# Kernel tuning notes

Hardware: AMD Instinct MI355X
Metric: run time of the kernel (lower is better)

## Reference

```python
import jax, jax.numpy as jnp
import numpy as np

NUM_EMBEDDINGS = 16384
EMBED_DIM = 256
COMMITMENT_COST = 0.25  # legacy=True: vq_loss = commit + beta * codebook


def setup_inputs() -> dict:
    key = jax.random.key(0)
    k1, k2, k3, k4 = jax.random.split(key, 4)
    z = jax.random.normal(k1, (8, 2048, EMBED_DIM), dtype=jnp.float32)
    # frozen codebook: normal(0, embedding_dim ** -0.5)
    codebook = jax.random.normal(k2, (NUM_EMBEDDINGS, EMBED_DIM), dtype=jnp.float32) * (EMBED_DIM ** -0.5)
    # learnable linear projection, torch default uniform init
    bound = 1.0 / np.sqrt(EMBED_DIM)
    proj_w = jax.random.uniform(k3, (EMBED_DIM, EMBED_DIM), dtype=jnp.float32, minval=-bound, maxval=bound)
    proj_b = jax.random.uniform(k4, (EMBED_DIM,), dtype=jnp.float32, minval=-bound, maxval=bound)
    return {"z": z, "codebook": codebook, "proj_w": proj_w, "proj_b": proj_b}


def reference(z, codebook, proj_w, proj_b):
    B, T, D = z.shape
    # projected codebook (the only learned part of the quantizer)
    quant_codebook = codebook @ proj_w.T + proj_b  # [K, D]
    z_flat = z.reshape(-1, D)  # [N, D]
    # squared L2 distances: ||z||^2 + ||c||^2 - 2 z.c
    dists = (
        jnp.sum(z_flat * z_flat, axis=1, keepdims=True)
        + jnp.sum(quant_codebook * quant_codebook, axis=1)
        - 2.0 * jnp.einsum("nd,kd->nk", z_flat, quant_codebook)
    )  # [N, K]
    idx = jnp.argmin(dists, axis=1)  # [N]
    quantized = quant_codebook[idx].reshape(z.shape)  # [B, T, D]

    commitment_loss = jnp.mean((jax.lax.stop_gradient(quantized) - z) ** 2)
    codebook_loss = jnp.mean((quantized - jax.lax.stop_gradient(z)) ** 2)
    vq_loss = commitment_loss + COMMITMENT_COST * codebook_loss  # legacy formulation

    # straight-through estimator
    quantized = z + jax.lax.stop_gradient(quantized - z)
    encoding_indices = idx.reshape(B, T)
    return quantized, vq_loss, encoding_indices
```

## Files before the change

### kernel.cpp

```cpp
#include <hip/hip_runtime.h>

typedef unsigned short u16;
typedef __bf16 bf16x8 __attribute__((ext_vector_type(8)));
typedef float f32x4 __attribute__((ext_vector_type(4)));

#define NQ 16384
#define NC 16384
#define DD 256
#define BM 128
#define BN 128
#define BK 64
#define NSPLIT 8
#define NPART (NSPLIT * 2)
#define NTILES ((NC / NSPLIT) / BN)

__device__ __forceinline__ u16 f2bf(float x) {
  unsigned u = __float_as_uint(x);
  u += 0x7fffu + ((u >> 16) & 1u);
  return (u16)(u >> 16);
}
__device__ __forceinline__ float bf2f(u16 h) {
  return __uint_as_float(((unsigned)h) << 16);
}

__device__ __forceinline__ void gl2lds16(const void* g, void* l) {
  __builtin_amdgcn_global_load_lds((__attribute__((address_space(1))) void*)g,
                                   (__attribute__((address_space(3))) void*)l,
                                   16, 0, 0);
}

__global__ __launch_bounds__(256) void split_z_kernel(const float* __restrict__ z,
                                                      u16* __restrict__ Ah,
                                                      u16* __restrict__ Al) {
  size_t i = (size_t)blockIdx.x * 256 + threadIdx.x;
  float4 v = ((const float4*)z)[i];
  float f[4] = {v.x, v.y, v.z, v.w};
  u16 hh[4], ll[4];
#pragma unroll
  for (int j = 0; j < 4; ++j) {
    hh[j] = f2bf(f[j]);
    ll[j] = f2bf(f[j] - bf2f(hh[j]));
  }
  ushort4 h; h.x = hh[0]; h.y = hh[1]; h.z = hh[2]; h.w = hh[3];
  ushort4 l; l.x = ll[0]; l.y = ll[1]; l.z = ll[2]; l.w = ll[3];
  ((ushort4*)Ah)[i] = h;
  ((ushort4*)Al)[i] = l;
}

__global__ __launch_bounds__(64) void norm256_kernel(const float* __restrict__ x,
                                                     float* __restrict__ nrm) {
  const int row = blockIdx.x * 64 + threadIdx.x;
  const float* p = x + (size_t)row * 256;
  float half[2];
#pragma unroll
  for (int h = 0; h < 2; ++h) {
    const float* q = p + h * 128;
    float r[8];
#pragma unroll
    for (int j = 0; j < 8; ++j) r[j] = __fmul_rn(q[j], q[j]);
    for (int i = 8; i < 128; i += 8)
#pragma unroll
      for (int j = 0; j < 8; ++j) r[j] = __fadd_rn(r[j], __fmul_rn(q[i + j], q[i + j]));
    half[h] = __fadd_rn(__fadd_rn(__fadd_rn(r[0], r[1]), __fadd_rn(r[2], r[3])),
                        __fadd_rn(__fadd_rn(r[4], r[5]), __fadd_rn(r[6], r[7])));
  }
  nrm[row] = __fadd_rn(half[0], half[1]);
}

__global__ __launch_bounds__(256) void qc_gemm_kernel(const float* __restrict__ cb,
                                                      const float* __restrict__ W,
                                                      const float* __restrict__ bias,
                                                      float* __restrict__ qc) {
  __shared__ float As[64][33];
  __shared__ float Bs[64][33];
  const int bm = blockIdx.x >> 2;
  const int bn = blockIdx.x & 3;
  const int m0 = bm * 64, n0 = bn * 64;
  const int t = threadIdx.x;
  const int tx = t & 15, ty = t >> 4;
  float acc[4][4] = {};
  for (int kc = 0; kc < 256; kc += 32) {
    __syncthreads();
#pragma unroll
    for (int j = 0; j < 8; ++j) {
      int idx = j * 256 + t;
      int r = idx >> 5, c = idx & 31;
      As[r][c] = cb[(size_t)(m0 + r) * 256 + kc + c];
      Bs[r][c] = W[(size_t)(n0 + r) * 256 + kc + c];
    }
    __syncthreads();
#pragma unroll
    for (int kk = 0; kk < 32; ++kk) {
      float a[4], b[4];
#pragma unroll
      for (int u = 0; u < 4; ++u) a[u] = As[ty * 4 + u][kk];
#pragma unroll
      for (int v = 0; v < 4; ++v) b[v] = Bs[tx * 4 + v][kk];
#pragma unroll
      for (int u = 0; u < 4; ++u)
#pragma unroll
        for (int v = 0; v < 4; ++v) acc[u][v] += a[u] * b[v];
    }
  }
#pragma unroll
  for (int u = 0; u < 4; ++u)
#pragma unroll
    for (int v = 0; v < 4; ++v) {
      int r = m0 + ty * 4 + u, c = n0 + tx * 4 + v;
      qc[(size_t)r * 256 + c] = acc[u][v] + bias[c];
    }
}

__global__ __launch_bounds__(256) void split_qc_kernel(const float* __restrict__ qc,
                                                       u16* __restrict__ Bh,
                                                       u16* __restrict__ Bl) {
  size_t i = (size_t)blockIdx.x * 256 + threadIdx.x;
  float4 v = ((const float4*)qc)[i];
  float f[4] = {v.x, v.y, v.z, v.w};
  u16 hh[4], ll[4];
#pragma unroll
  for (int j = 0; j < 4; ++j) {
    hh[j] = f2bf(f[j]);
    ll[j] = f2bf(f[j] - bf2f(hh[j]));
  }
  ushort4 h; h.x = hh[0]; h.y = hh[1]; h.z = hh[2]; h.w = hh[3];
  ushort4 l; l.x = ll[0]; l.y = ll[1]; l.z = ll[2]; l.w = ll[3];
  ((ushort4*)Bh)[i] = h;
  ((ushort4*)Bl)[i] = l;
}

__global__ __launch_bounds__(256, 2) void vq_argmin_kernel(
    const u16* __restrict__ Ah, const u16* __restrict__ Al,
    const u16* __restrict__ Bh, const u16* __restrict__ Bl,
    const float* __restrict__ cnorm, const float* __restrict__ znorm,
    float* __restrict__ pval, int* __restrict__ pidx) {
  __shared__ __align__(16) u16 Ahs[BM * BK];
  __shared__ __align__(16) u16 Als[BM * BK];
  __shared__ __align__(16) u16 Bhs[BN * BK];
  __shared__ __align__(16) u16 Bls[BN * BK];

  const int bm = blockIdx.x / NSPLIT;
  const int spl = blockIdx.x % NSPLIT;
  const int lane = threadIdx.x & 63;
  const int wid = threadIdx.x >> 6;
  const int wm = wid >> 1, wn = wid & 1;
  const int l15 = lane & 15;
  const int lg = lane >> 4;
  const int m0 = bm * BM;
  const int ns0 = spl * (NC / NSPLIT);

  const int st_r = lane >> 3;
  const int st_g = (lane & 7) * 8;

  float zrow[4][4];
#pragma unroll
  for (int mi = 0; mi < 4; ++mi)
#pragma unroll
    for (int i = 0; i < 4; ++i)
      zrow[mi][i] = znorm[m0 + wm * 64 + mi * 16 + lg * 4 + i];

  float rmin[4][4];
  int ridx[4][4];
#pragma unroll
  for (int a = 0; a < 4; ++a)
#pragma unroll
    for (int b = 0; b < 4; ++b) { rmin[a][b] = 3.4e38f; ridx[a][b] = 0; }

  for (int nt = 0; nt < NTILES; ++nt) {
    const int n0 = ns0 + nt * BN;
    f32x4 acc[4][4];
#pragma unroll
    for (int a = 0; a < 4; ++a)
#pragma unroll
      for (int b = 0; b < 4; ++b) {
        f32x4 zz = {0.f, 0.f, 0.f, 0.f};
        acc[a][b] = zz;
      }

    for (int kc = 0; kc < DD; kc += BK) {
      __syncthreads();
#pragma unroll
      for (int j = 0; j < 4; ++j) {
        const int grp = wid * 4 + j;
        const int o = grp * 512;
        const int r = grp * 8 + st_r;
        const size_t ga = (size_t)(m0 + r) * DD + kc + st_g;
        const size_t gb = (size_t)(n0 + r) * DD + kc + st_g;
        gl2lds16(Ah + ga, Ahs + o);
        gl2lds16(Al + ga, Als + o);
        gl2lds16(Bh + gb, Bhs + o);
        gl2lds16(Bl + gb, Bls + o);
      }
      __syncthreads();
#pragma unroll
      for (int ks = 0; ks < BK; ks += 32) {
        const int ko = ks + lg * 8;
        bf16x8 ah[4], al[4], bh[4], bl[4];
#pragma unroll
        for (int mi = 0; mi < 4; ++mi) {
          const int r = wm * 64 + mi * 16 + l15;
          ah[mi] = *(const bf16x8*)&Ahs[r * BK + ko];
          al[mi] = *(const bf16x8*)&Als[r * BK + ko];
        }
#pragma unroll
        for (int ni = 0; ni < 4; ++ni) {
          const int r = wn * 64 + ni * 16 + l15;
          bh[ni] = *(const bf16x8*)&Bhs[r * BK + ko];
          bl[ni] = *(const bf16x8*)&Bls[r * BK + ko];
        }
#pragma unroll
        for (int mi = 0; mi < 4; ++mi)
#pragma unroll
          for (int ni = 0; ni < 4; ++ni) {
            acc[mi][ni] = __builtin_amdgcn_mfma_f32_16x16x32_bf16(ah[mi], bh[ni], acc[mi][ni], 0, 0, 0);
            acc[mi][ni] = __builtin_amdgcn_mfma_f32_16x16x32_bf16(ah[mi], bl[ni], acc[mi][ni], 0, 0, 0);
            acc[mi][ni] = __builtin_amdgcn_mfma_f32_16x16x32_bf16(al[mi], bh[ni], acc[mi][ni], 0, 0, 0);
          }
      }
    }
#pragma unroll
    for (int ni = 0; ni < 4; ++ni) {
      const int col = n0 + wn * 64 + ni * 16 + l15;
      const float cn = cnorm[col];
#pragma unroll
      for (int mi = 0; mi < 4; ++mi)
#pragma unroll
        for (int i = 0; i < 4; ++i) {
          const float s = __fadd_rn(zrow[mi][i], cn);
          const float v = __fsub_rn(s, __fmul_rn(2.0f, acc[mi][ni][i]));
          if (v < rmin[mi][i]) { rmin[mi][i] = v; ridx[mi][i] = col; }
        }
    }
  }
#pragma unroll
  for (int mi = 0; mi < 4; ++mi)
#pragma unroll
    for (int i = 0; i < 4; ++i) {
      float v = rmin[mi][i];
      int ix = ridx[mi][i];
#pragma unroll
      for (int d = 1; d < 16; d <<= 1) {
        float ov = __shfl_xor(v, d);
        int oi = __shfl_xor(ix, d);
        if (ov < v || (ov == v && oi < ix)) { v = ov; ix = oi; }
      }
      if (l15 == 0) {
        const int row = m0 + wm * 64 + mi * 16 + lg * 4 + i;
        const int part = spl * 2 + wn;
        pval[(size_t)part * NQ + row] = v;
        pidx[(size_t)part * NQ + row] = ix;
      }
    }
}

__global__ __launch_bounds__(256) void finalize_kernel(
    const float* __restrict__ pval, const int* __restrict__ pidx,
    const float* __restrict__ qc, const float* __restrict__ z,
    float* __restrict__ out, float* __restrict__ loss_acc) {
  __shared__ int sidx[8];
  __shared__ float red[256];
  const int bid = blockIdx.x;
  const int t = threadIdx.x;
  if (t < 8) {
    const int row = bid * 8 + t;
    float best = pval[row];
    int bi = pidx[row];
    for (int s2 = 1; s2 < NPART; ++s2) {
      float v = pval[(size_t)s2 * NQ + row];
      int ix = pidx[(size_t)s2 * NQ + row];
      if (v < best || (v == best && ix < bi)) { best = v; bi = ix; }
    }
    sidx[t] = bi;
    out[4194305 + row] = (float)bi;
  }
  __syncthreads();
  float d2 = 0.f;
#pragma unroll
  for (int r = 0; r < 8; ++r) {
    const int row = bid * 8 + r;
    const int ix = sidx[r];
    const float q = qc[(size_t)ix * 256 + t];
    const float zz = z[(size_t)row * 256 + t];
    out[(size_t)row * 256 + t] = q;
    const float d = q - zz;
    d2 += d * d;
  }
  red[t] = d2;
  for (int st = 128; st; st >>= 1) {
    __syncthreads();
    if (t < st) red[t] += red[t + st];
  }
  if (t == 0) atomicAdd(loss_acc, red[0]);
}

__global__ void write_loss_kernel(const float* __restrict__ loss_acc, float* __restrict__ out) {
  out[4194304] = 1.25f * loss_acc[0] / 4194304.0f;
}

extern "C" void kernel_launch(void* const* d_in, const int* in_sizes, int n_in,
                              void* d_out, int out_size, void* d_ws, size_t ws_size,
                              hipStream_t stream) {
  const float* z = (const float*)d_in[0];
  const float* cb = (const float*)d_in[1];
  const float* W = (const float*)d_in[2];
  const float* bias = (const float*)d_in[3];
  float* out = (float*)d_out;
  char* ws = (char*)d_ws;

  constexpr size_t OFF_QC = 0;
  constexpr size_t OFF_AH = OFF_QC + 16777216;
  constexpr size_t OFF_AL = OFF_AH + 8388608;
  constexpr size_t OFF_BH = OFF_AL + 8388608;
  constexpr size_t OFF_BL = OFF_BH + 8388608;
  constexpr size_t OFF_CN = OFF_BL + 8388608;
  constexpr size_t OFF_ZN = OFF_CN + 65536;
  constexpr size_t OFF_PV = OFF_ZN + 65536;
  constexpr size_t OFF_PI = OFF_PV + 1048576;
  constexpr size_t OFF_ACC = OFF_PI + 1048576;

  float* qc = (float*)(ws + OFF_QC);
  u16* Ah = (u16*)(ws + OFF_AH);
  u16* Al = (u16*)(ws + OFF_AL);
  u16* Bh = (u16*)(ws + OFF_BH);
  u16* Bl = (u16*)(ws + OFF_BL);
  float* cn = (float*)(ws + OFF_CN);
  float* zn = (float*)(ws + OFF_ZN);
  float* pv = (float*)(ws + OFF_PV);
  int* pi = (int*)(ws + OFF_PI);
  float* lacc = (float*)(ws + OFF_ACC);

  hipMemsetAsync(lacc, 0, 4, stream);
  split_z_kernel<<<4096, 256, 0, stream>>>(z, Ah, Al);
  qc_gemm_kernel<<<1024, 256, 0, stream>>>(cb, W, bias, qc);
  norm256_kernel<<<NQ / 64, 64, 0, stream>>>(z, zn);
  norm256_kernel<<<NC / 64, 64, 0, stream>>>(qc, cn);
  split_qc_kernel<<<4096, 256, 0, stream>>>(qc, Bh, Bl);
  vq_argmin_kernel<<<(NQ / BM) * NSPLIT, 256, 0, stream>>>(Ah, Al, Bh, Bl, cn, zn, pv, pi);
  finalize_kernel<<<NQ / 8, 256, 0, stream>>>(pv, pi, qc, z, out, lacc);
  write_loss_kernel<<<1, 1, 0, stream>>>(lacc, out);
}
```

Before: 582.1 us.

## XOR-swizzle LDS tiles in argmin GEMM and parallelize row norms across lanes

The argmin kernel now stores and reads each 16-byte chunk of the A/B tiles in LDS at a position XOR'd with the row index. This spreads the bf16x8 fragment reads of 16 consecutive rows across banks, where the 128-byte row stride previously made them conflict. The norm kernel now gives each row to 8 lanes with strided loads and shuffle reductions, instead of one thread walking a 1KB row with poor coalescing. The norm summation order changes, which can slightly alter rounding and could flip argmin ties.

```diff
diff --git a/kernel.cpp b/kernel.cpp
--- a/kernel.cpp
+++ b/kernel.cpp
@@ -47,24 +47,28 @@
   ((ushort4*)Al)[i] = l;
 }
 
-__global__ __launch_bounds__(64) void norm256_kernel(const float* __restrict__ x,
-                                                     float* __restrict__ nrm) {
-  const int row = blockIdx.x * 64 + threadIdx.x;
-  const float* p = x + (size_t)row * 256;
+__global__ __launch_bounds__(256) void norm256_kernel(const float* __restrict__ x,
+                                                      float* __restrict__ nrm) {
+  const int t = threadIdx.x;
+  const int j = t & 7;
+  const int row = blockIdx.x * 32 + (t >> 3);
+  const float* q = x + (size_t)row * 256;
   float half[2];
 #pragma unroll
   for (int h = 0; h < 2; ++h) {
-    const float* q = p + h * 128;
-    float r[8];
-#pragma unroll
-    for (int j = 0; j < 8; ++j) r[j] = __fmul_rn(q[j], q[j]);
-    for (int i = 8; i < 128; i += 8)
-#pragma unroll
-      for (int j = 0; j < 8; ++j) r[j] = __fadd_rn(r[j], __fmul_rn(q[i + j], q[i + j]));
-    half[h] = __fadd_rn(__fadd_rn(__fadd_rn(r[0], r[1]), __fadd_rn(r[2], r[3])),
-                        __fadd_rn(__fadd_rn(r[4], r[5]), __fadd_rn(r[6], r[7])));
-  }
-  nrm[row] = __fadd_rn(half[0], half[1]);
+    const float* p = q + h * 128;
+    float v0 = p[j];
+    float r = __fmul_rn(v0, v0);
+#pragma unroll
+    for (int i = 8; i < 128; i += 8) {
+      float v = p[i + j];
+      r = __fadd_rn(r, __fmul_rn(v, v));
+    }
+    float s1 = __fadd_rn(r, __shfl_xor(r, 1));
+    float s2 = __fadd_rn(s1, __shfl_xor(s1, 2));
+    half[h] = __fadd_rn(s2, __shfl_xor(s2, 4));
+  }
+  if (j == 0) nrm[row] = __fadd_rn(half[0], half[1]);
 }
 
 __global__ __launch_bounds__(256) void qc_gemm_kernel(const float* __restrict__ cb,
@@ -150,7 +154,7 @@
   const int ns0 = spl * (NC / NSPLIT);
 
   const int st_r = lane >> 3;
-  const int st_g = (lane & 7) * 8;
+  const int st_g = (((lane & 7) ^ (lane >> 3)) << 3);
 
   float zrow[4][4];
 #pragma unroll
@@ -194,19 +198,21 @@
       __syncthreads();
 #pragma unroll
       for (int ks = 0; ks < BK; ks += 32) {
-        const int ko = ks + lg * 8;
+        const int c = (ks >> 3) + lg;
         bf16x8 ah[4], al[4], bh[4], bl[4];
 #pragma unroll
         for (int mi = 0; mi < 4; ++mi) {
           const int r = wm * 64 + mi * 16 + l15;
-          ah[mi] = *(const bf16x8*)&Ahs[r * BK + ko];
-          al[mi] = *(const bf16x8*)&Als[r * BK + ko];
+          const int off = r * BK + ((c ^ (r & 7)) << 3);
+          ah[mi] = *(const bf16x8*)&Ahs[off];
+          al[mi] = *(const bf16x8*)&Als[off];
         }
 #pragma unroll
         for (int ni = 0; ni < 4; ++ni) {
           const int r = wn * 64 + ni * 16 + l15;
-          bh[ni] = *(const bf16x8*)&Bhs[r * BK + ko];
-          bl[ni] = *(const bf16x8*)&Bls[r * BK + ko];
+          const int off = r * BK + ((c ^ (r & 7)) << 3);
+          bh[ni] = *(const bf16x8*)&Bhs[off];
+          bl[ni] = *(const bf16x8*)&Bls[off];
         }
 #pragma unroll
         for (int mi = 0; mi < 4; ++mi)
@@ -332,8 +338,8 @@
   hipMemsetAsync(lacc, 0, 4, stream);
   split_z_kernel<<<4096, 256, 0, stream>>>(z, Ah, Al);
   qc_gemm_kernel<<<1024, 256, 0, stream>>>(cb, W, bias, qc);
-  norm256_kernel<<<NQ / 64, 64, 0, stream>>>(z, zn);
-  norm256_kernel<<<NC / 64, 64, 0, stream>>>(qc, cn);
+  norm256_kernel<<<NQ / 32, 256, 0, stream>>>(z, zn);
+  norm256_kernel<<<NC / 32, 256, 0, stream>>>(qc, cn);
   split_qc_kernel<<<4096, 256, 0, stream>>>(qc, Bh, Bl);
   vq_argmin_kernel<<<(NQ / BM) * NSPLIT, 256, 0, stream>>>(Ah, Al, Bh, Bl, cn, zn, pv, pi);
   finalize_kernel<<<NQ / 8, 256, 0, stream>>>(pv, pi, qc, z, out, lacc);
```

After: 549.9 us. 5.5% less time.
